# Kernel optimization log

Measured on AMD Instinct MI355X. Metric: run time of the kernel, lower is better.

Reference implementation:

```python
import jax, jax.numpy as jnp
import numpy as np

# --- basis bookkeeping (mirrors TwoBodyToSpherical._generate_buffers) ---
METADATA = np.array([3, 2, 1], dtype=np.int64)          # shells per l
N_IRREPS = 2 * np.arange(3, dtype=np.int64) + 1          # 2l+1
REP_OFFSETS = np.concatenate([[0], np.cumsum(METADATA * N_IRREPS)[:-1]])
NUM_REPS_1D = int((METADATA * N_IRREPS).sum())           # = 14
M_IDX_MAP = {0: [0], 1: [0, 2, 1], 2: [0, 1, 2, 3, 4]}
ANGULAR = {"s": 0, "p": 1, "d": 2}

C_AOS = ["1s", "2s", "3s"] + ["2p"] * 3 + ["3p"] * 3 + ["3d"] * 5
H_AOS = ["1s", "2s"]


def _build_repid_map(aos):
    # faithful port of the per-element repid_map construction (valence_only=True)
    repid = np.zeros(len(aos), dtype=np.int64)
    dst_n, l_last, m_qc = 0, 0, 0
    for i, ao in enumerate(aos):
        l = ANGULAR[ao[1]]
        if l > l_last:
            dst_n = 0
        repid[i] = REP_OFFSETS[l] + dst_n + M_IDX_MAP[l][m_qc] * METADATA[l]
        if m_qc == 2 * l:
            m_qc = 0
            dst_n += 1
        else:
            m_qc += 1
        l_last = l
    return repid


def setup_inputs() -> dict:
    key = jax.random.key(0)
    maps = {"C": _build_repid_map(C_AOS), "H": _build_repid_map(H_AOS)}
    atomsybs = ["C"] * 400 + ["H"] * 100               # 500 atoms
    n_atoms = len(atomsybs)
    dst_rep_ids_1d = np.concatenate([maps[a] for a in atomsybs])
    lens = np.array([len(maps[a]) for a in atomsybs], dtype=np.int64)
    dst_offsets_1d = np.repeat(np.arange(n_atoms, dtype=np.int64), lens)
    dst_flat_ids_1d = dst_offsets_1d * NUM_REPS_1D + dst_rep_ids_1d  # [N_ao]=5800
    n_ao = dst_flat_ids_1d.shape[0]
    feat_ten = jax.random.normal(key, (n_ao, n_ao), dtype=jnp.float32)
    return {
        "feat_ten": feat_ten,
        "dst_flat_ids_1d": jnp.asarray(dst_flat_ids_1d, dtype=jnp.int32),
        "n_atoms": n_atoms,
        "num_reps_1d": NUM_REPS_1D,
    }


def reference(feat_ten, dst_flat_ids_1d, n_atoms, num_reps_1d):
    total = n_atoms * num_reps_1d                        # 7000
    # 2D destination flat ids: outer-sum of 1D ids (rep_dims=(0,1))
    ids2d = (dst_flat_ids_1d[:, None] * total + dst_flat_ids_1d[None, :]).reshape(-1)
    flat = feat_ten.reshape(-1)
    out_flat = jnp.zeros((total * total,), dtype=feat_ten.dtype).at[ids2d].add(flat)
    # view(n_atoms, R, n_atoms, R) then transpose(1,2) -> [A, A, R, R]
    out = out_flat.reshape(n_atoms, num_reps_1d, n_atoms, num_reps_1d)
    return jnp.transpose(out, (0, 2, 1, 3))
```

## Files before the change

kernel.cpp:

```cpp
#include <hip/hip_runtime.h>

constexpr int R = 14;
constexpr int A = 500;
constexpr int TOTAL = A * R;
constexpr int TILE = R * R;
constexpr long long OUT_SIZE = (long long)TOTAL * TOTAL;

__global__ void init_inv_kernel(int* __restrict__ inv) {
    int t = blockIdx.x * blockDim.x + threadIdx.x;
    if (t < TOTAL) inv[t] = -1;
}

__global__ void build_inv_kernel(const int* __restrict__ dst, int n_ao,
                                 int* __restrict__ inv) {
    int t = blockIdx.x * blockDim.x + threadIdx.x;
    if (t < n_ao) inv[dst[t]] = t;
}

__global__ void gather_kernel(const float* __restrict__ feat,
                              const int* __restrict__ inv,
                              float* __restrict__ out,
                              int n_ao) {
    long long base = ((long long)blockIdx.x * blockDim.x + threadIdx.x) * 4;
    if (base >= OUT_SIZE) return;

    int tile = (int)(base / TILE);
    int e    = (int)(base % TILE);
    int a1 = tile / A;
    int a2 = tile - a1 * A;
    const int* __restrict__ inv1 = inv + a1 * R;
    const int* __restrict__ inv2 = inv + a2 * R;

    float4 v;
    float* vp = &v.x;
#pragma unroll
    for (int k = 0; k < 4; ++k) {
        int ee = e + k;
        int r1 = ee / R;
        int r2 = ee - r1 * R;
        int i = inv1[r1];
        int j = inv2[r2];
        float val = 0.0f;
        if ((i | j) >= 0)
            val = feat[i * n_ao + j];
        vp[k] = val;
    }
    *reinterpret_cast<float4*>(out + base) = v;
}

extern "C" void kernel_launch(void* const* d_in, const int* in_sizes, int n_in,
                              void* d_out, int out_size, void* d_ws, size_t ws_size,
                              hipStream_t stream) {
    const float* feat = (const float*)d_in[0];
    const int*   dst  = (const int*)d_in[1];
    int n_ao = in_sizes[1];

    int* inv = (int*)d_ws;

    init_inv_kernel<<<(TOTAL + 255) / 256, 256, 0, stream>>>(inv);
    build_inv_kernel<<<(n_ao + 255) / 256, 256, 0, stream>>>(dst, n_ao, inv);

    long long nthreads = OUT_SIZE / 4;
    int blocks = (int)((nthreads + 255) / 256);
    gather_kernel<<<blocks, 256, 0, stream>>>(feat, inv, (float*)d_out, n_ao);
}
```

Baseline: 351.5 us.

## Stage per-atom feature rows in shared memory and emit output tiles per atom group

Replaces the flat per-element gather with a block-per-(atom, group of 25 atoms) kernel. Each block loads the contiguous feature rows of atom a1 over the column span of the group into LDS, then writes the group's output tiles from shared memory using precomputed per-atom row offsets and permutation maps. This cuts the scattered global reads and the per-element inverse-map lookups. It adds an extra small precompute kernel, and it assumes each atom's AOs are contiguous and that the group's column span fits in the padded buffer.

Result: no change. 356.6 us (+1.5%).

```diff
diff --git a/kernel.cpp b/kernel.cpp
--- a/kernel.cpp
+++ b/kernel.cpp
@@ -4,7 +4,11 @@
 constexpr int A = 500;
 constexpr int TOTAL = A * R;
 constexpr int TILE = R * R;
-constexpr long long OUT_SIZE = (long long)TOTAL * TOTAL;
+constexpr int G = 25;
+constexpr int NG = A / G;
+constexpr int MAXW = G * R;
+constexpr int WP = MAXW + 3;
+constexpr int CHUNK = G * TILE;
 
 __global__ void init_inv_kernel(int* __restrict__ inv) {
     int t = blockIdx.x * blockDim.x + threadIdx.x;
@@ -17,35 +21,77 @@
     if (t < n_ao) inv[dst[t]] = t;
 }
 
-__global__ void gather_kernel(const float* __restrict__ feat,
-                              const int* __restrict__ inv,
-                              float* __restrict__ out,
-                              int n_ao) {
-    long long base = ((long long)blockIdx.x * blockDim.x + threadIdx.x) * 4;
-    if (base >= OUT_SIZE) return;
+__global__ void atom_info_kernel(const int* __restrict__ inv,
+                                 int* __restrict__ arow,
+                                 int* __restrict__ ncols,
+                                 int* __restrict__ pm) {
+    int a = blockIdx.x * blockDim.x + threadIdx.x;
+    if (a >= A) return;
+    int lo = 0x7fffffff, hi = -1;
+#pragma unroll
+    for (int r = 0; r < R; ++r) {
+        int v = inv[a * R + r];
+        if (v >= 0) { lo = min(lo, v); hi = max(hi, v); }
+    }
+    arow[a] = lo;
+    ncols[a] = hi - lo + 1;
+#pragma unroll
+    for (int r = 0; r < R; ++r) {
+        int v = inv[a * R + r];
+        pm[a * R + r] = (v >= 0) ? (v - lo) : -1;
+    }
+}
 
-    int tile = (int)(base / TILE);
-    int e    = (int)(base % TILE);
-    int a1 = tile / A;
-    int a2 = tile - a1 * A;
-    const int* __restrict__ inv1 = inv + a1 * R;
-    const int* __restrict__ inv2 = inv + a2 * R;
+__global__ __launch_bounds__(256) void tile_kernel(
+        const float* __restrict__ feat,
+        const int* __restrict__ arow,
+        const int* __restrict__ ncols,
+        const int* __restrict__ pm,
+        float* __restrict__ out, int n_ao) {
+    const int g  = blockIdx.x % NG;
+    const int a1 = blockIdx.x / NG;
+    const int g0 = g * G;
+    const int tid = threadIdx.x;
 
-    float4 v;
-    float* vp = &v.x;
+    __shared__ float buf[R][WP];
+    __shared__ int s_pr[R];
+    __shared__ int s_pc[G * R];
+    __shared__ int s_off[G];
+
+    const int arow1 = arow[a1];
+    const int n1    = ncols[a1];
+    const int colL  = arow[g0];
+    const int W     = arow[g0 + G - 1] + ncols[g0 + G - 1] - colL;
+
+    for (int t = tid; t < G * R; t += 256) s_pc[t] = pm[g0 * R + t];
+    if (tid < R) s_pr[tid] = pm[a1 * R + tid];
+    if (tid < G) s_off[tid] = arow[g0 + tid] - colL;
+
+    for (int d = 0; d < n1; ++d) {
+        const float* src = feat + (long long)(arow1 + d) * n_ao + colL;
+        for (int c = tid; c < W; c += 256) buf[d][c] = src[c];
+    }
+    __syncthreads();
+
+    const long long outbase = ((long long)a1 * A + g0) * (long long)TILE;
+    for (int o4 = tid * 4; o4 < CHUNK; o4 += 1024) {
+        float4 v;
+        float* vp = &v.x;
 #pragma unroll
-    for (int k = 0; k < 4; ++k) {
-        int ee = e + k;
-        int r1 = ee / R;
-        int r2 = ee - r1 * R;
-        int i = inv1[r1];
-        int j = inv2[r2];
-        float val = 0.0f;
-        if ((i | j) >= 0)
-            val = feat[i * n_ao + j];
-        vp[k] = val;
+        for (int k = 0; k < 4; ++k) {
+            int o   = o4 + k;
+            int a2i = o / TILE;
+            int e   = o - a2i * TILE;
+            int r1  = e / R;
+            int r2  = e - r1 * R;
+            int d   = s_pr[r1];
+            int c   = s_pc[a2i * R + r2];
+            float val = 0.0f;
+            if ((d | c) >= 0) val = buf[d][s_off[a2i] + c];
+            vp[k] = val;
+        }
+        *reinterpret_cast<float4*>(out + outbase + o4) = v;
     }
-    *reinterpret_cast<float4*>(out + base) = v;
 }
 
 extern "C" void kernel_launch(void* const* d_in, const int* in_sizes, int n_in,
@@ -55,12 +101,15 @@
     const int*   dst  = (const int*)d_in[1];
     int n_ao = in_sizes[1];
 
-    int* inv = (int*)d_ws;
+    int* inv   = (int*)d_ws;
+    int* arow  = inv + TOTAL;
+    int* ncols = arow + A;
+    int* pm    = ncols + A;
 
     init_inv_kernel<<<(TOTAL + 255) / 256, 256, 0, stream>>>(inv);
     build_inv_kernel<<<(n_ao + 255) / 256, 256, 0, stream>>>(dst, n_ao, inv);
+    atom_info_kernel<<<(A + 255) / 256, 256, 0, stream>>>(inv, arow, ncols, pm);
 
-    long long nthreads = OUT_SIZE / 4;
-    int blocks = (int)((nthreads + 255) / 256);
-    gather_kernel<<<blocks, 256, 0, stream>>>(feat, inv, (float*)d_out, n_ao);
+    tile_kernel<<<A * NG, 256, 0, stream>>>(feat, arow, ncols, pm,
+                                            (float*)d_out, n_ao);
 }
```
